# Optimization experiments

Hardware: AMD Instinct MI355X
Metric: run time of the kernel (lower is better)

The kernel has to match this reference:

```python
import jax, jax.numpy as jnp
import numpy as np

N_SPECIES = 4
NUM_MODELS = 8
LAYER_DIMS = [384, 160, 128, 96, 1]
CELU_ALPHA = 0.1
N_ATOMS = 50000  # divisible by N_SPECIES -> balanced routing


def setup_inputs() -> dict:
    key = jax.random.key(0)
    ks = jax.random.split(key, 2 + 2 * (len(LAYER_DIMS) - 1))
    # Balanced species assignment: exactly N_ATOMS/N_SPECIES atoms per species,
    # randomly permuted (mirrors a real molecule's scattered per-species atoms
    # while keeping per-species group sizes static for jit).
    base = jnp.tile(jnp.arange(N_SPECIES, dtype=jnp.int64), N_ATOMS // N_SPECIES)
    species = jax.random.permutation(ks[0], base)[None, :]  # [1, N_ATOMS]
    aev = jax.random.normal(ks[1], (1, N_ATOMS, LAYER_DIMS[0]), dtype=jnp.float32)
    inp = {"species": species, "aev": aev}
    # Fused ensemble params per species: W [S, M, in, out], b [S, M, 1, out]
    for li in range(len(LAYER_DIMS) - 1):
        fin, fout = LAYER_DIMS[li], LAYER_DIMS[li + 1]
        scale = 1.0 / np.sqrt(fin)
        inp[f"W{li+1}"] = jax.random.uniform(
            ks[2 + 2 * li], (N_SPECIES, NUM_MODELS, fin, fout),
            dtype=jnp.float32, minval=-scale, maxval=scale)
        inp[f"b{li+1}"] = jax.random.uniform(
            ks[3 + 2 * li], (N_SPECIES, NUM_MODELS, 1, fout),
            dtype=jnp.float32, minval=-scale, maxval=scale)
    return inp


def _ensemble_mlp(x, W1, b1, W2, b2, W3, b3, W4, b4):
    # x: [S, n, F] routed atoms per species; W: [S, M, fin, fout]; b: [S, M, 1, fout]
    celu = lambda h: jax.nn.celu(h, alpha=CELU_ALPHA)
    h = celu(jnp.einsum('snf,smfo->smno', x, W1) + b1)   # [S, M, n, 160]
    h = celu(jnp.einsum('smnf,smfo->smno', h, W2) + b2)  # [S, M, n, 128]
    h = celu(jnp.einsum('smnf,smfo->smno', h, W3) + b3)  # [S, M, n, 96]
    h = jnp.einsum('smnf,smfo->smno', h, W4) + b4        # [S, M, n, 1]
    return h.mean(axis=1)                                 # mean over models -> [S, n, 1]


def reference(species, aev, W1, b1, W2, b2, W3, b3, W4, b4):
    n_atoms = species.shape[1]
    n_per = n_atoms // N_SPECIES
    # species-routed gather: stable argsort groups atoms by species; counts are
    # static (balanced) so reshape into [S, n_per] groups (== per-species index_select)
    order = jnp.argsort(species.reshape(-1), stable=True)
    x = aev.reshape(n_atoms, -1)[order].reshape(N_SPECIES, n_per, -1)
    atom_e = _ensemble_mlp(x, W1, b1, W2, b2, W3, b3, W4, b4)  # [S, n_per, 1]
    mol_energies = jnp.sum(atom_e).reshape(1)  # scatter-sum over all atoms/species
    return mol_energies
```

## Files before the change

kernel.cpp:

```cpp
#include <hip/hip_runtime.h>


#define NSP 4
#define NMODELS 8
#define MPB NMODELS
#define NATOMS 50000
#define NPER (NATOMS / NSP)
#define NPAD 12544
#define D0 384
#define D1 160
#define D2 128
#define D3 96
#define NRBLK ((NATOMS + 255) / 256)
#define ABLK 128
#define BPS ((NPER + ABLK - 1) / ABLK)
#define FRAGS_SM 184
#define CHUNKS_M 23
#define TOT_CHUNKS (MPB * CHUNKS_M)

typedef float f32x4 __attribute__((ext_vector_type(4)));
typedef __bf16 bf16x8 __attribute__((ext_vector_type(8)));

#define MFMA16(a, b, c) __builtin_amdgcn_mfma_f32_16x16x32_bf16((a), (b), (c), 0, 0, 0)

#define PALL_BYTES ((size_t)NSP * NMODELS * FRAGS_SM * 1024)
#define PBIAS_OFF PALL_BYTES
#define PBIAS_BYTES ((size_t)NSP * NMODELS * 512 * 2)
#define ORDER_OFF (PBIAS_OFF + PBIAS_BYTES)
#define BCNT_OFF (ORDER_OFF + (size_t)NATOMS * 4)
#define BPFX_OFF (BCNT_OFF + (size_t)NRBLK * NSP * 4)
#define BASE_OFF (BPFX_OFF + (size_t)NRBLK * NSP * 4)
#define AEVB_OFF (BASE_OFF + 1024)
#define AEVB_BYTES ((size_t)NSP * NPAD * D0 * 2)

static __device__ __forceinline__ unsigned short bfbits(float f) {
  __bf16 h = (__bf16)f;
  return __builtin_bit_cast(unsigned short, h);
}

static __device__ __forceinline__ float celu01(float x) {
  return fmaxf(x, 0.f) + 0.1f * fminf(0.f, __expf(x * 10.f) - 1.f);
}

static __device__ __forceinline__ void gload16(const void* g, void* l) {
  __builtin_amdgcn_global_load_lds(
      (const __attribute__((address_space(1))) unsigned int*)g,
      (__attribute__((address_space(3))) unsigned int*)l, 16, 0, 0);
}

__global__ __launch_bounds__(256) void count_kernel(const int* __restrict__ species,
                                                    int* __restrict__ bcnt) {
  __shared__ int cnt[NSP];
  int t = threadIdx.x;
  if (t < NSP) cnt[t] = 0;
  __syncthreads();
  int i = blockIdx.x * 256 + t;
  if (i < NATOMS) atomicAdd(&cnt[species[i]], 1);
  __syncthreads();
  if (t < NSP) bcnt[blockIdx.x * NSP + t] = cnt[t];
}

__global__ __launch_bounds__(256) void scan_kernel(const int* __restrict__ bcnt,
                                                   int* __restrict__ bpfx,
                                                   int* __restrict__ base) {
  int w = threadIdx.x >> 6;
  int lane = threadIdx.x & 63;
  __shared__ int totals[NSP];
  int carry = 0;
  for (int c = 0; c < (NRBLK + 63) / 64; ++c) {
    int idx = c * 64 + lane;
    int v = (idx < NRBLK) ? bcnt[idx * NSP + w] : 0;
    int incl = v;
    for (int off = 1; off < 64; off <<= 1) {
      int tv = __shfl_up(incl, off);
      if (lane >= off) incl += tv;
    }
    if (idx < NRBLK) bpfx[idx * NSP + w] = carry + incl - v;
    carry += __shfl(incl, 63);
  }
  if (lane == 0) totals[w] = carry;
  __syncthreads();
  if (threadIdx.x == 0) {
    int run = 0;
    for (int s = 0; s < NSP; ++s) { base[s] = run; run += totals[s]; }
  }
}

__global__ __launch_bounds__(256) void route_kernel(const int* __restrict__ species,
                                                    const int* __restrict__ bpfx,
                                                    const int* __restrict__ base,
                                                    int* __restrict__ order) {
  __shared__ int sp[256];
  int t = threadIdx.x;
  int i = blockIdx.x * 256 + t;
  sp[t] = (i < NATOMS) ? species[i] : -1;
  __syncthreads();
  if (i < NATOMS) {
    int s = sp[t];
    int rank = 0;
    for (int j = 0; j < t; ++j) rank += (sp[j] == s) ? 1 : 0;
    order[base[s] + bpfx[blockIdx.x * NSP + s] + rank] = i;
  }
}

__global__ __launch_bounds__(256) void aev_pack(const float* __restrict__ aev,
                                                const int* __restrict__ order,
                                                unsigned short* __restrict__ aevb) {
  int tid = blockIdx.x * 256 + threadIdx.x;
  const int perRow = D0 / 8;
  int row = tid / perRow;
  int seg = tid - row * perRow;
  if (row >= NSP * NPAD) return;
  int s = row / NPAD;
  int slot = row - s * NPAD;
  unsigned short o[8];
  if (slot < NPER) {
    int src = order[s * NPER + slot];
    const float4* q = (const float4*)(aev + (size_t)src * D0 + seg * 8);
    float4 v0 = q[0], v1 = q[1];
    o[0] = bfbits(v0.x); o[1] = bfbits(v0.y); o[2] = bfbits(v0.z); o[3] = bfbits(v0.w);
    o[4] = bfbits(v1.x); o[5] = bfbits(v1.y); o[6] = bfbits(v1.z); o[7] = bfbits(v1.w);
  } else {
#pragma unroll
    for (int e = 0; e < 8; ++e) o[e] = 0;
  }
  *(int4*)(aevb + (size_t)row * D0 + seg * 8) = *(const int4*)o;
}

__global__ __launch_bounds__(256) void pack_kernel(const float* __restrict__ W,
                                                   unsigned* __restrict__ dst,
                                                   int K, int N, int NT, int fragBase,
                                                   int total) {
  int tid = blockIdx.x * 256 + threadIdx.x;
  if (tid >= total) return;
  int per_sm = K * N / 2;
  int smi = tid / per_sm;
  int rem = tid - smi * per_sm;
  int frag = rem >> 8;
  int wi = rem & 255;
  int l = wi >> 2, d = wi & 3;
  int kf = frag / NT;
  int nt = frag - kf * NT;
  int k = kf * 32 + ((l >> 4) << 3) + 2 * d;
  int n = nt * 16 + (l & 15);
  const float* p = W + ((size_t)smi * K + k) * N + n;
  unsigned lo = bfbits(p[0]);
  unsigned hi = bfbits(p[N]);
  dst[((size_t)smi * FRAGS_SM + fragBase + frag) * 256 + wi] = lo | (hi << 16);
}

__global__ __launch_bounds__(256) void param_pack(const float* __restrict__ b1,
                                                  const float* __restrict__ b2,
                                                  const float* __restrict__ b3,
                                                  const float* __restrict__ W4,
                                                  const float* __restrict__ b4,
                                                  unsigned short* __restrict__ dst) {
  int i = blockIdx.x * 256 + threadIdx.x;
  if (i >= NSP * NMODELS * 512) return;
  int smi = i >> 9, o = i & 511;
  unsigned short v = 0;
  if (o < 160) v = bfbits(b1[smi * 160 + o]);
  else if (o < 288) v = bfbits(b2[smi * 128 + (o - 160)]);
  else if (o < 384) v = bfbits(b3[smi * 96 + (o - 288)]);
  else if (o < 480) v = bfbits(W4[smi * 96 + (o - 384)]);
  else if (o < 482) {
    unsigned u = __builtin_bit_cast(unsigned, b4[smi]);
    v = (unsigned short)((o == 480) ? (u & 0xffffu) : (u >> 16));
  }
  dst[i] = v;
}

#define CHUNK_HDR()                                                      \
  do {                                                                   \
    asm volatile("s_waitcnt vmcnt(2)" ::: "memory");                     \
    __builtin_amdgcn_s_barrier();                                        \
    const char* _src = wsrc + (size_t)tn * 8192;                         \
    char* _d = (char*)stage + wb_off + w * 2048;                         \
    gload16(_src, _d);                                                   \
    gload16(_src + 1024, _d + 1024);                                     \
    tn = (tn + 1 == TOT_CHUNKS) ? 0 : (tn + 1);                          \
    wb_off = (wb_off == 16384u) ? 0u : (wb_off + 8192u);                 \
  } while (0)

#define CHUNK_END() rb_off = (rb_off == 16384u) ? 0u : (rb_off + 8192u)

__global__ __launch_bounds__(256, 2) void mlp_kernel(
    const unsigned short* __restrict__ aevb,
    const unsigned short* __restrict__ pAll, const unsigned short* __restrict__ pPar,
    float* __restrict__ out) {
  __shared__ alignas(16) unsigned short stage[3][4096];
  __shared__ alignas(16) __bf16 hbuf[4][32][168];
  __shared__ alignas(16) unsigned short hpar[MPB * 512];

  const int nwg = NSP * BPS;
  const int cpx = nwg / 8;
  const int blk = (blockIdx.x % 8) * cpx + blockIdx.x / 8;
  const int s = blk / BPS;
  const int sb = blk - s * BPS;
  const int m0 = (blockIdx.x >> 3) & 7;
  const int tid = threadIdx.x;
  const int w = tid >> 6;
  const int l = tid & 63;
  const int l15 = l & 15;
  const int l4 = l >> 4;

  {
    const int4* src = (const int4*)(pPar + (size_t)s * NMODELS * 512);
    ((int4*)hpar)[tid] = src[tid];
    ((int4*)hpar)[tid + 256] = src[tid + 256];
  }

  const size_t smBase = (size_t)s * NMODELS * FRAGS_SM;
  const char* wsrc = (const char*)pAll + smBase * 1024 + (size_t)w * 2048 + (size_t)l * 16;

  bf16x8 a1[2][12];
#pragma unroll
  for (int mt = 0; mt < 2; ++mt) {
    int row = s * NPAD + sb * ABLK + w * 32 + mt * 16 + l15;
    const bf16x8* rp = (const bf16x8*)(aevb + (size_t)row * D0 + l4 * 8);
#pragma unroll
    for (int kf = 0; kf < 12; ++kf) a1[mt][kf] = rp[kf * 4];
  }

  const __bf16* hb = (const __bf16*)hpar;
  float acc4[2][4] = {{0.f, 0.f, 0.f, 0.f}, {0.f, 0.f, 0.f, 0.f}};
  float bbacc = 0.f;

  __syncthreads();

  const int c0 = m0 * CHUNKS_M;
  int tn = c0 + 2;
  unsigned rb_off = 0, wb_off = 16384u;
  {
    char* d0 = (char*)stage + w * 2048;
    const char* s0 = wsrc + (size_t)c0 * 8192;
    gload16(s0, d0);
    gload16(s0 + 1024, d0 + 1024);
    char* d1 = (char*)stage + 8192 + w * 2048;
    const char* s1 = wsrc + (size_t)(c0 + 1) * 8192;
    gload16(s1, d1);
    gload16(s1 + 1024, d1 + 1024);
  }

#pragma unroll 1
  for (int mi = 0; mi < MPB; ++mi) {
    const int m = (m0 + mi) & 7;
    f32x4 C[2][10];

#pragma unroll
    for (int mt = 0; mt < 2; ++mt)
#pragma unroll
      for (int nt = 0; nt < 10; ++nt) {
        f32x4 z; z[0] = z[1] = z[2] = z[3] = 0.f; C[mt][nt] = z;
      }
#pragma unroll
    for (int c = 0; c < 15; ++c) {
      CHUNK_HDR();
      const bf16x8* sbuf = (const bf16x8*)((const char*)stage + rb_off);
#pragma unroll
      for (int j = 0; j < 8; ++j) {
        const int f = c * 8 + j;
        bf16x8 b = sbuf[j * 64 + l];
        C[0][f % 10] = MFMA16(a1[0][f / 10], b, C[0][f % 10]);
        C[1][f % 10] = MFMA16(a1[1][f / 10], b, C[1][f % 10]);
      }
      CHUNK_END();
    }
#pragma unroll
    for (int nt = 0; nt < 10; ++nt) {
      float bias = (float)hb[m * 512 + nt * 16 + l15];
#pragma unroll
      for (int mt = 0; mt < 2; ++mt)
#pragma unroll
        for (int r = 0; r < 4; ++r)
          hbuf[w][mt * 16 + l4 * 4 + r][nt * 16 + l15] = (__bf16)celu01(C[mt][nt][r] + bias);
    }

    bf16x8 a2[2][5];
#pragma unroll
    for (int mt = 0; mt < 2; ++mt)
#pragma unroll
      for (int kf = 0; kf < 5; ++kf)
        a2[mt][kf] = *(const bf16x8*)&hbuf[w][mt * 16 + l15][kf * 32 + l4 * 8];

#pragma unroll
    for (int mt = 0; mt < 2; ++mt)
#pragma unroll
      for (int nt = 0; nt < 8; ++nt) {
        f32x4 z; z[0] = z[1] = z[2] = z[3] = 0.f; C[mt][nt] = z;
      }
#pragma unroll
    for (int lc = 0; lc < 5; ++lc) {
      CHUNK_HDR();
      const bf16x8* sbuf = (const bf16x8*)((const char*)stage + rb_off);
#pragma unroll
      for (int j = 0; j < 8; ++j) {
        bf16x8 b = sbuf[j * 64 + l];
        C[0][j] = MFMA16(a2[0][lc], b, C[0][j]);
        C[1][j] = MFMA16(a2[1][lc], b, C[1][j]);
      }
      CHUNK_END();
    }
#pragma unroll
    for (int nt = 0; nt < 8; ++nt) {
      float bias = (float)hb[m * 512 + 160 + nt * 16 + l15];
#pragma unroll
      for (int mt = 0; mt < 2; ++mt)
#pragma unroll
        for (int r = 0; r < 4; ++r)
          hbuf[w][mt * 16 + l4 * 4 + r][nt * 16 + l15] = (__bf16)celu01(C[mt][nt][r] + bias);
    }

    bf16x8 a3[2][4];
#pragma unroll
    for (int mt = 0; mt < 2; ++mt)
#pragma unroll
      for (int kf = 0; kf < 4; ++kf)
        a3[mt][kf] = *(const bf16x8*)&hbuf[w][mt * 16 + l15][kf * 32 + l4 * 8];

#pragma unroll
    for (int mt = 0; mt < 2; ++mt)
#pragma unroll
      for (int nt = 0; nt < 6; ++nt) {
        f32x4 z; z[0] = z[1] = z[2] = z[3] = 0.f; C[mt][nt] = z;
      }
#pragma unroll
    for (int lc = 0; lc < 3; ++lc) {
      CHUNK_HDR();
      const bf16x8* sbuf = (const bf16x8*)((const char*)stage + rb_off);
#pragma unroll
      for (int j = 0; j < 8; ++j) {
        const int f = lc * 8 + j;
        bf16x8 b = sbuf[j * 64 + l];
        C[0][f % 6] = MFMA16(a3[0][f / 6], b, C[0][f % 6]);
        C[1][f % 6] = MFMA16(a3[1][f / 6], b, C[1][f % 6]);
      }
      CHUNK_END();
    }

    float e[2][4] = {{0.f, 0.f, 0.f, 0.f}, {0.f, 0.f, 0.f, 0.f}};
#pragma unroll
    for (int nt = 0; nt < 6; ++nt) {
      float b3v = (float)hb[m * 512 + 288 + nt * 16 + l15];
      float w4v = (float)hb[m * 512 + 384 + nt * 16 + l15];
#pragma unroll
      for (int mt = 0; mt < 2; ++mt)
#pragma unroll
        for (int r = 0; r < 4; ++r)
          e[mt][r] += celu01(C[mt][nt][r] + b3v) * w4v;
    }
#pragma unroll
    for (int mt = 0; mt < 2; ++mt)
#pragma unroll
      for (int r = 0; r < 4; ++r) acc4[mt][r] += e[mt][r];
    bbacc += ((const float*)hpar)[m * 256 + 240];
  }

  asm volatile("s_waitcnt vmcnt(0)" ::: "memory");

  float tot = 0.f;
#pragma unroll
  for (int mt = 0; mt < 2; ++mt)
#pragma unroll
    for (int r = 0; r < 4; ++r) {
      float v = acc4[mt][r];
      v += __shfl_xor(v, 1);
      v += __shfl_xor(v, 2);
      v += __shfl_xor(v, 4);
      v += __shfl_xor(v, 8);
      int slot = sb * ABLK + w * 32 + mt * 16 + l4 * 4 + r;
      if (l15 == 0 && slot < NPER) tot += v + bbacc;
    }
  tot *= (1.f / NMODELS);
#pragma unroll
  for (int off = 1; off < 64; off <<= 1) tot += __shfl_xor(tot, off);
  if (l == 0) atomicAdd(out, tot);
}

extern "C" void kernel_launch(void* const* d_in, const int* in_sizes, int n_in,
                              void* d_out, int out_size, void* d_ws, size_t ws_size,
                              hipStream_t stream) {
  (void)in_sizes; (void)n_in; (void)out_size; (void)ws_size;
  const int* species = (const int*)d_in[0];
  const float* aev = (const float*)d_in[1];
  const float* W1 = (const float*)d_in[2];
  const float* b1 = (const float*)d_in[3];
  const float* W2 = (const float*)d_in[4];
  const float* b2 = (const float*)d_in[5];
  const float* W3 = (const float*)d_in[6];
  const float* b3 = (const float*)d_in[7];
  const float* W4 = (const float*)d_in[8];
  const float* b4 = (const float*)d_in[9];
  float* out = (float*)d_out;
  char* ws = (char*)d_ws;

  unsigned short* pAll = (unsigned short*)ws;
  unsigned short* pPar = (unsigned short*)(ws + PBIAS_OFF);
  int* order = (int*)(ws + ORDER_OFF);
  int* bcnt = (int*)(ws + BCNT_OFF);
  int* bpfx = (int*)(ws + BPFX_OFF);
  int* base = (int*)(ws + BASE_OFF);
  unsigned short* aevb = (unsigned short*)(ws + AEVB_OFF);

  hipMemsetAsync(d_out, 0, sizeof(float), stream);

  count_kernel<<<NRBLK, 256, 0, stream>>>(species, bcnt);
  scan_kernel<<<1, 256, 0, stream>>>(bcnt, bpfx, base);
  route_kernel<<<NRBLK, 256, 0, stream>>>(species, bpfx, base, order);

  {
    int total = NSP * NPAD * (D0 / 8);
    aev_pack<<<total / 256, 256, 0, stream>>>(aev, order, aevb);
  }
  {
    int total = NSP * NMODELS * D0 * D1 / 2;
    pack_kernel<<<(total + 255) / 256, 256, 0, stream>>>(W1, (unsigned*)pAll, D0, D1, D1 / 16, 0, total);
  }
  {
    int total = NSP * NMODELS * D1 * D2 / 2;
    pack_kernel<<<(total + 255) / 256, 256, 0, stream>>>(W2, (unsigned*)pAll, D1, D2, D2 / 16, 120, total);
  }
  {
    int total = NSP * NMODELS * D2 * D3 / 2;
    pack_kernel<<<(total + 255) / 256, 256, 0, stream>>>(W3, (unsigned*)pAll, D2, D3, D3 / 16, 160, total);
  }
  {
    int total = NSP * NMODELS * 512;
    param_pack<<<(total + 255) / 256, 256, 0, stream>>>(b1, b2, b3, W4, b4, pPar);
  }

  mlp_kernel<<<NSP * BPS, 256, 0, stream>>>(aevb, pAll, pPar, out);
}
```

Measured before the change: 194.8 us.

## Double atom block per workgroup to 512 threads sharing staged weight chunks

Each workgroup now handles 256 atoms with 8 waves instead of 128 atoms with 4. Each 8 KB weight chunk staged in LDS is then shared by twice as many waves, so every wave issues one 16-byte load per chunk instead of two, and the waitcnt depth is adjusted to match. The grid is halved, and the XCD-aware block remap is rewritten to handle a block count not divisible by 8. The costs are fewer workgroups, a larger LDS footprint, and a heavier barrier per chunk.

Measured after the change: 215.9 us. +10.8%, slower.

```diff
diff --git a/kernel.cpp b/kernel.cpp
--- a/kernel.cpp
+++ b/kernel.cpp
@@ -12,7 +12,7 @@
 #define D2 128
 #define D3 96
 #define NRBLK ((NATOMS + 255) / 256)
-#define ABLK 128
+#define ABLK 256
 #define BPS ((NPER + ABLK - 1) / ABLK)
 #define FRAGS_SM 184
 #define CHUNKS_M 23
@@ -172,32 +172,31 @@
 
 #define CHUNK_HDR()                                                      \
   do {                                                                   \
-    asm volatile("s_waitcnt vmcnt(2)" ::: "memory");                     \
+    asm volatile("s_waitcnt vmcnt(1)" ::: "memory");                     \
     __builtin_amdgcn_s_barrier();                                        \
-    const char* _src = wsrc + (size_t)tn * 8192;                         \
-    char* _d = (char*)stage + wb_off + w * 2048;                         \
-    gload16(_src, _d);                                                   \
-    gload16(_src + 1024, _d + 1024);                                     \
+    gload16(wsrc + (size_t)tn * 8192, (char*)stage + wb_off + w * 1024); \
     tn = (tn + 1 == TOT_CHUNKS) ? 0 : (tn + 1);                          \
     wb_off = (wb_off == 16384u) ? 0u : (wb_off + 8192u);                 \
   } while (0)
 
 #define CHUNK_END() rb_off = (rb_off == 16384u) ? 0u : (rb_off + 8192u)
 
-__global__ __launch_bounds__(256, 2) void mlp_kernel(
+__global__ __launch_bounds__(512, 2) void mlp_kernel(
     const unsigned short* __restrict__ aevb,
     const unsigned short* __restrict__ pAll, const unsigned short* __restrict__ pPar,
     float* __restrict__ out) {
   __shared__ alignas(16) unsigned short stage[3][4096];
-  __shared__ alignas(16) __bf16 hbuf[4][32][168];
+  __shared__ alignas(16) __bf16 hbuf[8][32][168];
   __shared__ alignas(16) unsigned short hpar[MPB * 512];
 
-  const int nwg = NSP * BPS;
-  const int cpx = nwg / 8;
-  const int blk = (blockIdx.x % 8) * cpx + blockIdx.x / 8;
+  const int orig = blockIdx.x;
+  const int xcd = orig & 7;
+  const int pos = orig >> 3;
+  const int q = (NSP * BPS) / 8, r = (NSP * BPS) & 7;
+  const int blk = ((xcd < r) ? xcd * (q + 1) : r * (q + 1) + (xcd - r) * q) + pos;
   const int s = blk / BPS;
   const int sb = blk - s * BPS;
-  const int m0 = (blockIdx.x >> 3) & 7;
+  const int m0 = pos & 7;
   const int tid = threadIdx.x;
   const int w = tid >> 6;
   const int l = tid & 63;
@@ -207,11 +206,10 @@
   {
     const int4* src = (const int4*)(pPar + (size_t)s * NMODELS * 512);
     ((int4*)hpar)[tid] = src[tid];
-    ((int4*)hpar)[tid + 256] = src[tid + 256];
   }
 
   const size_t smBase = (size_t)s * NMODELS * FRAGS_SM;
-  const char* wsrc = (const char*)pAll + smBase * 1024 + (size_t)w * 2048 + (size_t)l * 16;
+  const char* wsrc = (const char*)pAll + smBase * 1024 + (size_t)w * 1024 + (size_t)l * 16;
 
   bf16x8 a1[2][12];
 #pragma unroll
@@ -231,16 +229,8 @@
   const int c0 = m0 * CHUNKS_M;
   int tn = c0 + 2;
   unsigned rb_off = 0, wb_off = 16384u;
-  {
-    char* d0 = (char*)stage + w * 2048;
-    const char* s0 = wsrc + (size_t)c0 * 8192;
-    gload16(s0, d0);
-    gload16(s0 + 1024, d0 + 1024);
-    char* d1 = (char*)stage + 8192 + w * 2048;
-    const char* s1 = wsrc + (size_t)(c0 + 1) * 8192;
-    gload16(s1, d1);
-    gload16(s1 + 1024, d1 + 1024);
-  }
+  gload16(wsrc + (size_t)c0 * 8192, (char*)stage + w * 1024);
+  gload16(wsrc + (size_t)(c0 + 1) * 8192, (char*)stage + 8192 + w * 1024);
 
 #pragma unroll 1
   for (int mi = 0; mi < MPB; ++mi) {
@@ -272,8 +262,8 @@
 #pragma unroll
       for (int mt = 0; mt < 2; ++mt)
 #pragma unroll
-        for (int r = 0; r < 4; ++r)
-          hbuf[w][mt * 16 + l4 * 4 + r][nt * 16 + l15] = (__bf16)celu01(C[mt][nt][r] + bias);
+        for (int r2 = 0; r2 < 4; ++r2)
+          hbuf[w][mt * 16 + l4 * 4 + r2][nt * 16 + l15] = (__bf16)celu01(C[mt][nt][r2] + bias);
     }
 
     bf16x8 a2[2][5];
@@ -307,8 +297,8 @@
 #pragma unroll
       for (int mt = 0; mt < 2; ++mt)
 #pragma unroll
-        for (int r = 0; r < 4; ++r)
-          hbuf[w][mt * 16 + l4 * 4 + r][nt * 16 + l15] = (__bf16)celu01(C[mt][nt][r] + bias);
+        for (int r2 = 0; r2 < 4; ++r2)
+          hbuf[w][mt * 16 + l4 * 4 + r2][nt * 16 + l15] = (__bf16)celu01(C[mt][nt][r2] + bias);
     }
 
     bf16x8 a3[2][4];
@@ -346,13 +336,13 @@
 #pragma unroll
       for (int mt = 0; mt < 2; ++mt)
 #pragma unroll
-        for (int r = 0; r < 4; ++r)
-          e[mt][r] += celu01(C[mt][nt][r] + b3v) * w4v;
-    }
-#pragma unroll
-    for (int mt = 0; mt < 2; ++mt)
-#pragma unroll
-      for (int r = 0; r < 4; ++r) acc4[mt][r] += e[mt][r];
+        for (int r2 = 0; r2 < 4; ++r2)
+          e[mt][r2] += celu01(C[mt][nt][r2] + b3v) * w4v;
+    }
+#pragma unroll
+    for (int mt = 0; mt < 2; ++mt)
+#pragma unroll
+      for (int r2 = 0; r2 < 4; ++r2) acc4[mt][r2] += e[mt][r2];
     bbacc += ((const float*)hpar)[m * 256 + 240];
   }
 
@@ -362,13 +352,13 @@
 #pragma unroll
   for (int mt = 0; mt < 2; ++mt)
 #pragma unroll
-    for (int r = 0; r < 4; ++r) {
-      float v = acc4[mt][r];
+    for (int r2 = 0; r2 < 4; ++r2) {
+      float v = acc4[mt][r2];
       v += __shfl_xor(v, 1);
       v += __shfl_xor(v, 2);
       v += __shfl_xor(v, 4);
       v += __shfl_xor(v, 8);
-      int slot = sb * ABLK + w * 32 + mt * 16 + l4 * 4 + r;
+      int slot = sb * ABLK + w * 32 + mt * 16 + l4 * 4 + r2;
       if (l15 == 0 && slot < NPER) tot += v + bbacc;
     }
   tot *= (1.f / NMODELS);
@@ -429,5 +419,5 @@
     param_pack<<<(total + 255) / 256, 256, 0, stream>>>(b1, b2, b3, W4, b4, pPar);
   }
 
-  mlp_kernel<<<NSP * BPS, 256, 0, stream>>>(aevb, pAll, pPar, out);
-}
+  mlp_kernel<<<NSP * BPS, 512, 0, stream>>>(aevb, pAll, pPar, out);
+}
```
